# Kernel optimization log

Hardware: AMD Instinct MI355X
Metric: run time of the kernel (lower is better)

The kernel has to match this reference:

```python
import math
import jax, jax.numpy as jnp
import numpy as np
from jax import lax

PATCHSIZE = [(8, 8), (4, 4), (2, 2), (1, 1)]  # (width, height)
BN_EPS = 1e-5


def setup_inputs() -> dict:
    key = jax.random.key(0)
    ks = jax.random.split(key, 6)
    b, c, h, w = 4, 256, 64, 64
    s = 1.0 / math.sqrt(c)
    return {
        "x": jax.random.normal(ks[0], (b, c, h, w), jnp.float32),
        "Wq": jax.random.normal(ks[1], (c, c), jnp.float32) * s,
        "bq": jnp.zeros((c,), jnp.float32),
        "Wk": jax.random.normal(ks[2], (c, c), jnp.float32) * s,
        "bk": jnp.zeros((c,), jnp.float32),
        "Wv": jax.random.normal(ks[3], (c, c), jnp.float32) * s,
        "bv": jnp.zeros((c,), jnp.float32),
        "Wo": jax.random.normal(ks[4], (c, c, 3, 3), jnp.float32) * (1.0 / math.sqrt(c * 9)),
        "bo": jnp.zeros((c,), jnp.float32),
        "gamma": jnp.ones((c,), jnp.float32),
        "beta": jnp.zeros((c,), jnp.float32),
        "running_mean": jnp.zeros((c,), jnp.float32),
        "running_var": jnp.ones((c,), jnp.float32),
    }


def _patch_attention(q, k, v, ph, pw):
    # q/k/v: [b, dk, h, w] -> tokens [b, n_patches, dk*ph*pw]
    b, dk, h, w = q.shape
    oh, ow = h // ph, w // pw

    def to_tok(t):
        t = t.reshape(b, dk, oh, ph, ow, pw)
        return t.transpose(0, 2, 4, 1, 3, 5).reshape(b, oh * ow, dk * ph * pw)

    qt, kt, vt = to_tok(q), to_tok(k), to_tok(v)
    scale = 1.0 / math.sqrt(dk * ph * pw)
    scores = jnp.einsum("bnd,bmd->bnm", qt, kt) * scale
    y = jnp.einsum("bnm,bmd->bnd", jax.nn.softmax(scores, axis=-1), vt)
    y = y.reshape(b, oh, ow, dk, ph, pw).transpose(0, 3, 1, 4, 2, 5)
    return y.reshape(b, dk, h, w)


def reference(x, Wq, bq, Wk, bk, Wv, bv, Wo, bo, gamma, beta, running_mean, running_var):
    b, c, h, w = x.shape
    nh = len(PATCHSIZE)
    dk = c // nh
    # 1x1 conv QKV projections
    q = jnp.einsum("bchw,oc->bohw", x, Wq) + bq[:, None, None]
    k = jnp.einsum("bchw,oc->bohw", x, Wk) + bk[:, None, None]
    v = jnp.einsum("bchw,oc->bohw", x, Wv) + bv[:, None, None]
    outs = []
    for i, (pw_, ph_) in enumerate(PATCHSIZE):
        sl = slice(i * dk, (i + 1) * dk)
        outs.append(_patch_attention(q[:, sl], k[:, sl], v[:, sl], ph_, pw_))
    out = jnp.concatenate(outs, axis=1)
    # 3x3 conv, SAME padding
    out = lax.conv_general_dilated(
        out, Wo, window_strides=(1, 1), padding="SAME",
        dimension_numbers=("NCHW", "OIHW", "NCHW"),
    ) + bo[:, None, None]
    # BatchNorm2d (inference-mode with running stats)
    inv = lax.rsqrt(running_var + BN_EPS)
    out = (out - running_mean[:, None, None]) * (gamma * inv)[:, None, None] + beta[:, None, None]
    # LeakyReLU(0.2)
    return jnp.where(out >= 0, out, 0.2 * out)
```

## Files before the change

kernel.cpp:

```cpp
#include <hip/hip_runtime.h>
#include <hip/hip_bf16.h>
#include <math.h>

#define NPOS 4096
#define CPB  1048576
#define QOFF  ((size_t)0)
#define KOFF  ((size_t)4194304)
#define VOFF  ((size_t)8388608)
#define AOFF  ((size_t)12582912)
#define S0OFF ((size_t)16777216)
#define WTOFF ((size_t)21250048)
#define QTOFF   S0OFF
#define KTOFF   (S0OFF + (size_t)2097152)
#define SP0OFF  (S0OFF + (size_t)4194304)
#define VTOFF   QOFF
#define ML3OFF  (QOFF + (size_t)2097152)
#define ML2OFF  (QOFF + (size_t)2228224)
#define OP3OFF  KOFF
#define SP1OFF  VOFF
#define OP2OFF  (VOFF + (size_t)2097152)

#define LOG2E 1.44269504088896340736f

typedef __attribute__((ext_vector_type(8))) short bf16x8;
typedef __attribute__((ext_vector_type(4))) float f32x4;

static __device__ __forceinline__ unsigned short f2bf(float f) {
  __hip_bfloat16 h = __float2bfloat16(f);
  unsigned short u;
  __builtin_memcpy(&u, &h, sizeof(u));
  return u;
}

static __device__ __forceinline__ float bf2f(unsigned short u) {
  unsigned v = ((unsigned)u) << 16;
  float f;
  __builtin_memcpy(&f, &v, sizeof(f));
  return f;
}

template<int PH, int PW>
__device__ __forceinline__ void scat_qk(unsigned short* __restrict__ dst,
                                        const unsigned short* __restrict__ Ac,
                                        int gh, int tid) {
  constexpr int PP = PH * PW, OW = 64 / PW, D = 64 * PP;
  int po = gh / PH, y = gh % PH;
  constexpr int NCH = 64 * OW;
#pragma unroll
  for (int j = 0; j < NCH / 256; ++j) {
    int id = j * 256 + tid;
    int c = id / OW, qo = id % OW;
    int tt = po * OW + qo;
    unsigned short buf[PW];
#pragma unroll
    for (int x = 0; x < PW; ++x) buf[x] = Ac[c * 66 + qo * PW + x];
    unsigned short* dp = &dst[(size_t)tt * D + c * PP + y * PW];
    if constexpr (PW == 8)      { uint4 v;  __builtin_memcpy(&v, buf, 16); *(uint4*)dp = v; }
    else if constexpr (PW == 4) { uint2 v;  __builtin_memcpy(&v, buf, 8);  *(uint2*)dp = v; }
    else                        { unsigned v; __builtin_memcpy(&v, buf, 4); *(unsigned*)dp = v; }
  }
}

template<int PH, int PW>
__device__ __forceinline__ void scat_v(unsigned short* __restrict__ dst,
                                       const unsigned short* __restrict__ Ac,
                                       int gh, int tid) {
  constexpr int PP = PH * PW, OW = 64 / PW, NT = 4096 / PP;
  int po = gh / PH, y = gh % PH;
  constexpr int NCH = 64 * PW;
  constexpr int CPT = (NCH + 255) / 256;
#pragma unroll
  for (int j = 0; j < CPT; ++j) {
    int id = j * 256 + tid;
    if (NCH < 256 && id >= NCH) break;
    int c = id / PW, x = id % PW;
    int d = c * PP + y * PW + x;
    unsigned short* dp = &dst[(size_t)d * NT + po * OW];
#pragma unroll
    for (int s = 0; s < OW; s += 8) {
      unsigned short buf[8];
#pragma unroll
      for (int e = 0; e < 8; ++e) buf[e] = Ac[c * 66 + (s + e) * PW + x];
      uint4 v; __builtin_memcpy(&v, buf, 16);
      *(uint4*)&dp[s] = v;
    }
  }
}

__global__ __launch_bounds__(256) void qkv_fused(
    const float* __restrict__ x,
    const float* __restrict__ Wq, const float* __restrict__ Wk, const float* __restrict__ Wv,
    const float* __restrict__ bq, const float* __restrict__ bk, const float* __restrict__ bv,
    const float* __restrict__ Wo, unsigned short* __restrict__ W2,
    unsigned short* __restrict__ qt, unsigned short* __restrict__ kt_,
    unsigned short* __restrict__ vt) {
  if (blockIdx.z == 12) {
    int o = blockIdx.y * 64 + blockIdx.x;
    size_t base = (size_t)o * 2304;
#pragma unroll
    for (int r = 0; r < 9; ++r) {
      int rr = r * 256 + threadIdx.x;
      int c = rr / 9, k = rr % 9;
      W2[(size_t)k * 65536 + (size_t)o * 256 + c] = f2bf(Wo[base + rr]);
    }
    return;
  }
  int b = blockIdx.z / 3, t = blockIdx.z % 3;
  const float* W    = (t == 0) ? Wq : (t == 1) ? Wk : Wv;
  const float* bias = (t == 0) ? bq : (t == 1) ? bk : bv;
  int h = blockIdx.y, gh = blockIdx.x;
  int o0 = h * 64, p0 = gh * 64;
  __shared__ unsigned short smem[2 * 64 * 72];
  unsigned short* Wt = smem;
  unsigned short* Xs = smem + 64 * 72;
  int tid = threadIdx.x;
  int wv = tid >> 6, l = tid & 63;
  int lg = l >> 4, ll = l & 15;
  f32x4 acc[4];
#pragma unroll
  for (int mi = 0; mi < 4; ++mi) acc[mi] = (f32x4){0.f, 0.f, 0.f, 0.f};

  int wol = tid >> 2, wcp = (tid & 3) * 16;
  int xcc = tid >> 6, xpz = tid & 63;

  for (int c0 = 0; c0 < 256; c0 += 64) {
    __syncthreads();
#pragma unroll
    for (int u = 0; u < 4; ++u) {
      float4 w4 = *(const float4*)&W[(size_t)(o0 + wol) * 256 + c0 + wcp + u * 4];
      ushort4 pk;
      pk.x = f2bf(w4.x); pk.y = f2bf(w4.y); pk.z = f2bf(w4.z); pk.w = f2bf(w4.w);
      *(ushort4*)&Wt[wol * 72 + wcp + u * 4] = pk;
    }
#pragma unroll
    for (int r = 0; r < 16; ++r) {
      int c = xcc * 16 + r;
      Xs[xpz * 72 + c] = f2bf(x[(size_t)b * CPB + (size_t)(c0 + c) * NPOS + p0 + xpz]);
    }
    __syncthreads();
#pragma unroll
    for (int ks = 0; ks < 2; ++ks) {
      bf16x8 xb = *(const bf16x8*)&Xs[(wv * 16 + ll) * 72 + ks * 32 + lg * 8];
#pragma unroll
      for (int mi = 0; mi < 4; ++mi) {
        bf16x8 wa = *(const bf16x8*)&Wt[(mi * 16 + ll) * 72 + ks * 32 + lg * 8];
        acc[mi] = __builtin_amdgcn_mfma_f32_16x16x32_bf16(wa, xb, acc[mi], 0, 0, 0);
      }
    }
  }
  __syncthreads();
  float qs = 1.0f;
  if (t == 0) qs = (h == 2) ? 0.0625f * LOG2E : (h == 3) ? 0.125f * LOG2E : 1.0f;
  unsigned short* Ac = smem;
#pragma unroll
  for (int mi = 0; mi < 4; ++mi)
#pragma unroll
    for (int r = 0; r < 4; ++r) {
      int ol = mi * 16 + lg * 4 + r;
      Ac[ol * 66 + wv * 16 + ll] = f2bf((acc[mi][r] + bias[o0 + ol]) * qs);
    }
  __syncthreads();
  if (t < 2) {
    unsigned short* dst = (t == 0 ? qt : kt_) + ((size_t)b * 4 + h) * 262144;
    switch (h) {
      case 0: scat_qk<8, 8>(dst, Ac, gh, tid); break;
      case 1: scat_qk<4, 4>(dst, Ac, gh, tid); break;
      case 2: scat_qk<2, 2>(dst, Ac, gh, tid); break;
      default: {
        int p = tid >> 2, c0 = (tid & 3) * 16;
        unsigned short buf[16];
#pragma unroll
        for (int e = 0; e < 16; ++e) buf[e] = Ac[(c0 + e) * 66 + p];
        uint4 v0, v1;
        __builtin_memcpy(&v0, buf, 16);
        __builtin_memcpy(&v1, buf + 8, 16);
        uint4* d4 = (uint4*)&dst[(size_t)(gh * 64 + p) * 64 + c0];
        d4[0] = v0; d4[1] = v1;
      } break;
    }
  } else {
    unsigned short* dst = vt + ((size_t)b * 4 + h) * 262144;
    switch (h) {
      case 0: scat_v<8, 8>(dst, Ac, gh, tid); break;
      case 1: scat_v<4, 4>(dst, Ac, gh, tid); break;
      case 2: scat_v<2, 2>(dst, Ac, gh, tid); break;
      default: {
        if (tid < 64) {
#pragma unroll
          for (int seg = 0; seg < 8; ++seg) {
            unsigned short buf[8];
#pragma unroll
            for (int e = 0; e < 8; ++e) buf[e] = Ac[tid * 66 + seg * 8 + e];
            uint4 v; __builtin_memcpy(&v, buf, 16);
            *(uint4*)&dst[(size_t)tid * 4096 + gh * 64 + seg * 8] = v;
          }
        }
      } break;
    }
  }
}

template<int NTOK, int DDIM, int NSPLIT, int KVB, int PH, int PW, int HEAD>
__device__ __forceinline__ void flash_body(
    unsigned char* smem, int b, int q0, int split,
    const unsigned short* __restrict__ qt, const unsigned short* __restrict__ kt_,
    const unsigned short* __restrict__ vt, unsigned short* __restrict__ opart,
    float* __restrict__ ml, unsigned short* __restrict__ attbf) {
  constexpr int KSTR = DDIM + 8;
  constexpr int VSTR = KVB + 4;
  constexpr int NT   = KVB / 16;
  constexpr int KCH  = DDIM / 32;
  constexpr int PKS  = KVB / 32;
  constexpr int OCG  = DDIM / 16;
  constexpr int PP = PH * PW, OW = 64 / PW;
  const unsigned short* Q = qt + ((size_t)b * 4 + HEAD) * 262144;
  const unsigned short* K = kt_ + ((size_t)b * 4 + HEAD) * 262144;
  const unsigned short* V = vt + ((size_t)b * 4 + HEAD) * 262144;
  unsigned short* Ks = (unsigned short*)smem;
  unsigned short* Vs = Ks + KVB * KSTR;
  unsigned short* Psw = Vs + DDIM * VSTR;
  int tid = threadIdx.x;
  int wv = tid >> 6, l = tid & 63;
  int lg = l >> 4, ll = l & 15;
  int qw = q0 + wv * 16;
  unsigned short* Ps = Psw + wv * 16 * VSTR;

  bf16x8 qf[KCH];
#pragma unroll
  for (int kc = 0; kc < KCH; ++kc)
    qf[kc] = *(const bf16x8*)&Q[(size_t)(qw + ll) * DDIM + kc * 32 + lg * 8];

  bf16x8 onesf;
#pragma unroll
  for (int e = 0; e < 8; ++e) onesf[e] = (short)0x3F80;

  f32x4 lacc = (f32x4){0.f, 0.f, 0.f, 0.f};
  f32x4 o_acc[OCG];
#pragma unroll
  for (int c = 0; c < OCG; ++c) o_acc[c] = (f32x4){0.f, 0.f, 0.f, 0.f};

  for (int kt0 = split * (NTOK / NSPLIT); kt0 < (split + 1) * (NTOK / NSPLIT); kt0 += KVB) {
    __syncthreads();
#pragma unroll
    for (int i = 0; i < KVB * DDIM / 2048; ++i) {
      int u = i * 256 + tid;
      int key = u / (DDIM / 8), part = u % (DDIM / 8);
      *(uint4*)&Ks[key * KSTR + part * 8] =
          *(const uint4*)&K[(size_t)(kt0 + key) * DDIM + part * 8];
    }
#pragma unroll
    for (int i = 0; i < KVB * DDIM / 2048; ++i) {
      int u = i * 256 + tid;
      int d = u / (KVB / 8), part = u % (KVB / 8);
      *(uint4*)&Vs[d * VSTR + part * 8] =
          *(const uint4*)&V[(size_t)d * NTOK + kt0 + part * 8];
    }
    __syncthreads();
    f32x4 s_acc[NT];
#pragma unroll
    for (int n = 0; n < NT; ++n) s_acc[n] = (f32x4){0.f, 0.f, 0.f, 0.f};
    __builtin_amdgcn_s_setprio(1);
#pragma unroll
    for (int n = 0; n < NT; ++n)
#pragma unroll
      for (int kc = 0; kc < KCH; ++kc) {
        bf16x8 kf = *(const bf16x8*)&Ks[(n * 16 + ll) * KSTR + kc * 32 + lg * 8];
        s_acc[n] = __builtin_amdgcn_mfma_f32_16x16x32_bf16(qf[kc], kf, s_acc[n], 0, 0, 0);
      }
    __builtin_amdgcn_s_setprio(0);
#pragma unroll
    for (int n = 0; n < NT; ++n)
#pragma unroll
      for (int r = 0; r < 4; ++r)
        Ps[(lg * 4 + r) * VSTR + n * 16 + ll] = f2bf(exp2f(s_acc[n][r]));
    __builtin_amdgcn_s_setprio(1);
#pragma unroll
    for (int pk = 0; pk < PKS; ++pk) {
      bf16x8 pa = *(const bf16x8*)&Ps[ll * VSTR + pk * 32 + lg * 8];
      lacc = __builtin_amdgcn_mfma_f32_16x16x32_bf16(pa, onesf, lacc, 0, 0, 0);
#pragma unroll
      for (int c = 0; c < OCG; ++c) {
        bf16x8 vf = *(const bf16x8*)&Vs[(c * 16 + ll) * VSTR + pk * 32 + lg * 8];
        o_acc[c] = __builtin_amdgcn_mfma_f32_16x16x32_bf16(pa, vf, o_acc[c], 0, 0, 0);
      }
    }
    __builtin_amdgcn_s_setprio(0);
  }
  if constexpr (NSPLIT > 1) {
    size_t ob = (size_t)(b * NSPLIT + split) * NTOK;
#pragma unroll
    for (int r = 0; r < 4; ++r) {
      int q = qw + lg * 4 + r;
#pragma unroll
      for (int c = 0; c < OCG; ++c)
        opart[(ob + q) * DDIM + c * 16 + ll] = f2bf(o_acc[c][r]);
      if (ll == 0) {
        ml[(ob + q) * 2]     = 0.f;
        ml[(ob + q) * 2 + 1] = lacc[r];
      }
    }
  } else {
#pragma unroll
    for (int r = 0; r < 4; ++r) {
      float inv = 1.0f / lacc[r];
      int q = qw + lg * 4 + r;
      int po = q / OW, qo = q % OW;
#pragma unroll
      for (int c = 0; c < OCG; ++c) {
        int d = c * 16 + ll;
        int ch = d / PP, rem = d % PP, y = rem / PW, x = rem % PW;
        int pos = (po * PH + y) * 64 + qo * PW + x;
        attbf[((size_t)b * NPOS + pos) * 256 + HEAD * 64 + ch] = f2bf(o_acc[c][r] * inv);
      }
    }
  }
}

__device__ __forceinline__ void flash3_dbuf(
    unsigned char* smem, int b, int q0, int split,
    const unsigned short* __restrict__ qt, const unsigned short* __restrict__ kt_,
    const unsigned short* __restrict__ vt, unsigned short* __restrict__ opart,
    float* __restrict__ ml) {
  const unsigned short* Q = qt + ((size_t)b * 4 + 3) * 262144;
  const unsigned short* K = kt_ + ((size_t)b * 4 + 3) * 262144;
  const unsigned short* V = vt + ((size_t)b * 4 + 3) * 262144;
  int tid = threadIdx.x;
  int wv = tid >> 6, l = tid & 63;
  int lg = l >> 4, ll = l & 15;
  int qwA = q0 + wv * 16;
  int qwB = qwA + 64;
  unsigned short* Ps = (unsigned short*)(smem + 18432) + wv * 16 * 72;

  bf16x8 qfA[2], qfB[2];
  qfA[0] = *(const bf16x8*)&Q[(size_t)(qwA + ll) * 64 + lg * 8];
  qfA[1] = *(const bf16x8*)&Q[(size_t)(qwA + ll) * 64 + 32 + lg * 8];
  qfB[0] = *(const bf16x8*)&Q[(size_t)(qwB + ll) * 64 + lg * 8];
  qfB[1] = *(const bf16x8*)&Q[(size_t)(qwB + ll) * 64 + 32 + lg * 8];

  bf16x8 onesf;
#pragma unroll
  for (int e = 0; e < 8; ++e) onesf[e] = (short)0x3F80;

  f32x4 laccA = (f32x4){0.f, 0.f, 0.f, 0.f};
  f32x4 laccB = (f32x4){0.f, 0.f, 0.f, 0.f};
  f32x4 o_accA[4], o_accB[4];
#pragma unroll
  for (int c = 0; c < 4; ++c) {
    o_accA[c] = (f32x4){0.f, 0.f, 0.f, 0.f};
    o_accB[c] = (f32x4){0.f, 0.f, 0.f, 0.f};
  }

  const int kstart = split * 1024, kend = kstart + 1024;

  {
    unsigned short* Kd = (unsigned short*)smem;
#pragma unroll
    for (int i = 0; i < 2; ++i) {
      int u = i * 256 + tid, row = u >> 3, part = u & 7;
      *(uint4*)&Kd[row * 72 + part * 8] =
          *(const uint4*)&K[(size_t)(kstart + row) * 64 + part * 8];
    }
  }
  __syncthreads();

  int cur = 0;
  for (int kt0 = kstart; kt0 < kend; kt0 += 64) {
    const bool more = (kt0 + 64) < kend;
    if (more) {
      unsigned short* Kd = (unsigned short*)(smem + (cur ^ 1) * 9216);
#pragma unroll
      for (int i = 0; i < 2; ++i) {
        int u = i * 256 + tid, row = u >> 3, part = u & 7;
        *(uint4*)&Kd[row * 72 + part * 8] =
            *(const uint4*)&K[(size_t)(kt0 + 64 + row) * 64 + part * 8];
      }
    }
    unsigned short* Kc = (unsigned short*)(smem + cur * 9216);

    bf16x8 vfr[2][4];
#pragma unroll
    for (int pk = 0; pk < 2; ++pk)
#pragma unroll
      for (int c = 0; c < 4; ++c)
        vfr[pk][c] = *(const bf16x8*)&V[(size_t)(c * 16 + ll) * 4096 + kt0 + pk * 32 + lg * 8];
    bf16x8 kfr[4][2];
#pragma unroll
    for (int n = 0; n < 4; ++n)
#pragma unroll
      for (int kc = 0; kc < 2; ++kc)
        kfr[n][kc] = *(const bf16x8*)&Kc[(n * 16 + ll) * 72 + kc * 32 + lg * 8];

    {
      f32x4 s_acc[4];
#pragma unroll
      for (int n = 0; n < 4; ++n) s_acc[n] = (f32x4){0.f, 0.f, 0.f, 0.f};
      __builtin_amdgcn_s_setprio(1);
#pragma unroll
      for (int n = 0; n < 4; ++n)
#pragma unroll
        for (int kc = 0; kc < 2; ++kc)
          s_acc[n] = __builtin_amdgcn_mfma_f32_16x16x32_bf16(qfA[kc], kfr[n][kc], s_acc[n],
                                                             0, 0, 0);
      __builtin_amdgcn_s_setprio(0);
#pragma unroll
      for (int n = 0; n < 4; ++n)
#pragma unroll
        for (int r = 0; r < 4; ++r)
          Ps[(lg * 4 + r) * 72 + n * 16 + ll] = f2bf(exp2f(s_acc[n][r]));
      __builtin_amdgcn_s_setprio(1);
#pragma unroll
      for (int pk = 0; pk < 2; ++pk) {
        bf16x8 pa = *(const bf16x8*)&Ps[ll * 72 + pk * 32 + lg * 8];
        laccA = __builtin_amdgcn_mfma_f32_16x16x32_bf16(pa, onesf, laccA, 0, 0, 0);
#pragma unroll
        for (int c = 0; c < 4; ++c)
          o_accA[c] = __builtin_amdgcn_mfma_f32_16x16x32_bf16(pa, vfr[pk][c], o_accA[c],
                                                              0, 0, 0);
      }
      __builtin_amdgcn_s_setprio(0);
    }
    {
      f32x4 s_acc[4];
#pragma unroll
      for (int n = 0; n < 4; ++n) s_acc[n] = (f32x4){0.f, 0.f, 0.f, 0.f};
      __builtin_amdgcn_s_setprio(1);
#pragma unroll
      for (int n = 0; n < 4; ++n)
#pragma unroll
        for (int kc = 0; kc < 2; ++kc)
          s_acc[n] = __builtin_amdgcn_mfma_f32_16x16x32_bf16(qfB[kc], kfr[n][kc], s_acc[n],
                                                             0, 0, 0);
      __builtin_amdgcn_s_setprio(0);
#pragma unroll
      for (int n = 0; n < 4; ++n)
#pragma unroll
        for (int r = 0; r < 4; ++r)
          Ps[(lg * 4 + r) * 72 + n * 16 + ll] = f2bf(exp2f(s_acc[n][r]));
      __builtin_amdgcn_s_setprio(1);
#pragma unroll
      for (int pk = 0; pk < 2; ++pk) {
        bf16x8 pa = *(const bf16x8*)&Ps[ll * 72 + pk * 32 + lg * 8];
        laccB = __builtin_amdgcn_mfma_f32_16x16x32_bf16(pa, onesf, laccB, 0, 0, 0);
#pragma unroll
        for (int c = 0; c < 4; ++c)
          o_accB[c] = __builtin_amdgcn_mfma_f32_16x16x32_bf16(pa, vfr[pk][c], o_accB[c],
                                                              0, 0, 0);
      }
      __builtin_amdgcn_s_setprio(0);
    }
    __syncthreads();
    cur ^= 1;
  }
  size_t ob = (size_t)(b * 4 + split) * 4096;
#pragma unroll
  for (int r = 0; r < 4; ++r) {
    int qA = qwA + lg * 4 + r;
    int qB = qwB + lg * 4 + r;
#pragma unroll
    for (int c = 0; c < 4; ++c) {
      opart[(ob + qA) * 64 + c * 16 + ll] = f2bf(o_accA[c][r]);
      opart[(ob + qB) * 64 + c * 16 + ll] = f2bf(o_accB[c][r]);
    }
    if (ll == 0) {
      ml[(ob + qA) * 2]     = 0.f;
      ml[(ob + qA) * 2 + 1] = laccA[r];
      ml[(ob + qB) * 2]     = 0.f;
      ml[(ob + qB) * 2 + 1] = laccB[r];
    }
  }
}

__device__ __forceinline__ void h0_score_body(unsigned char* smem, int b, int ds,
                                              const unsigned short* __restrict__ qt,
                                              const unsigned short* __restrict__ kt_,
                                              float* __restrict__ spart) {
  const unsigned short* Q = qt + ((size_t)b * 4 + 0) * 262144;
  const unsigned short* K = kt_ + ((size_t)b * 4 + 0) * 262144;
  unsigned short* Qc = (unsigned short*)smem;
  unsigned short* Kc = Qc + 64 * 72;
  int tid = threadIdx.x;
  int wv = tid >> 6, l = tid & 63;
  int lg = l >> 4, ll = l & 15;
  f32x4 s_acc[4];
#pragma unroll
  for (int n = 0; n < 4; ++n) s_acc[n] = (f32x4){0.f, 0.f, 0.f, 0.f};
  for (int ch = 0; ch < 8; ++ch) {
    int d0 = ds * 512 + ch * 64;
    __syncthreads();
#pragma unroll
    for (int i = 0; i < 2; ++i) {
      int u = i * 256 + tid, row = u >> 3, part = u & 7;
      *(uint4*)&Qc[row * 72 + part * 8] = *(const uint4*)&Q[(size_t)row * 4096 + d0 + part * 8];
      *(uint4*)&Kc[row * 72 + part * 8] = *(const uint4*)&K[(size_t)row * 4096 + d0 + part * 8];
    }
    __syncthreads();
#pragma unroll
    for (int n = 0; n < 4; ++n)
#pragma unroll
      for (int ks = 0; ks < 2; ++ks) {
        bf16x8 qa = *(const bf16x8*)&Qc[(wv * 16 + ll) * 72 + ks * 32 + lg * 8];
        bf16x8 kf = *(const bf16x8*)&Kc[(n * 16 + ll) * 72 + ks * 32 + lg * 8];
        s_acc[n] = __builtin_amdgcn_mfma_f32_16x16x32_bf16(qa, kf, s_acc[n], 0, 0, 0);
      }
  }
#pragma unroll
  for (int n = 0; n < 4; ++n)
#pragma unroll
    for (int r = 0; r < 4; ++r)
      spart[(((size_t)b * 8 + ds) * 64 + (wv * 16 + lg * 4 + r)) * 64 + n * 16 + ll] =
          s_acc[n][r];
}

__device__ __forceinline__ void h1_score_body(unsigned char* smem, int b, int qtile, int ds,
                                              const unsigned short* __restrict__ qt,
                                              const unsigned short* __restrict__ kt_,
                                              float* __restrict__ spart) {
  int q0 = qtile * 64, dbase = ds * 128;
  const unsigned short* Q = qt + ((size_t)b * 4 + 1) * 262144;
  const unsigned short* K = kt_ + ((size_t)b * 4 + 1) * 262144;
  unsigned short* Qc = (unsigned short*)smem;
  unsigned short* Kc = Qc + 64 * 72;
  int tid = threadIdx.x;
  int wv = tid >> 6, l = tid & 63;
  int lg = l >> 4, ll = l & 15;
  f32x4 s_acc[16];
#pragma unroll
  for (int n = 0; n < 16; ++n) s_acc[n] = (f32x4){0.f, 0.f, 0.f, 0.f};
  for (int dc = 0; dc < 2; ++dc) {
    int d0 = dbase + dc * 64;
    for (int kh = 0; kh < 2; ++kh) {
      __syncthreads();
      if (kh == 0) {
#pragma unroll
        for (int i = 0; i < 2; ++i) {
          int u = i * 256 + tid, row = u >> 3, part = u & 7;
          *(uint4*)&Qc[row * 72 + part * 8] =
              *(const uint4*)&Q[(size_t)(q0 + row) * 1024 + d0 + part * 8];
        }
      }
#pragma unroll
      for (int i = 0; i < 4; ++i) {
        int u = i * 256 + tid, row = u >> 3, part = u & 7;
        *(uint4*)&Kc[row * 72 + part * 8] =
            *(const uint4*)&K[(size_t)(kh * 128 + row) * 1024 + d0 + part * 8];
      }
      __syncthreads();
#pragma unroll
      for (int ks = 0; ks < 2; ++ks) {
        bf16x8 qa = *(const bf16x8*)&Qc[(wv * 16 + ll) * 72 + ks * 32 + lg * 8];
#pragma unroll
        for (int nn = 0; nn < 8; ++nn) {
          bf16x8 kf = *(const bf16x8*)&Kc[(nn * 16 + ll) * 72 + ks * 32 + lg * 8];
          s_acc[kh * 8 + nn] = __builtin_amdgcn_mfma_f32_16x16x32_bf16(qa, kf, s_acc[kh * 8 + nn],
                                                                      0, 0, 0);
        }
      }
    }
  }
#pragma unroll
  for (int n = 0; n < 16; ++n)
#pragma unroll
    for (int r = 0; r < 4; ++r) {
      int q = q0 + wv * 16 + lg * 4 + r;
      spart[(((size_t)b * 8 + ds) * 256 + q) * 256 + n * 16 + ll] = s_acc[n][r];
    }
}

__global__ __launch_bounds__(256) void attn_all(
    const unsigned short* __restrict__ qt, const unsigned short* __restrict__ kt_,
    const unsigned short* __restrict__ vt,
    unsigned short* __restrict__ op2, float* __restrict__ ml2,
    unsigned short* __restrict__ op3, float* __restrict__ ml3,
    float* __restrict__ sp0, float* __restrict__ sp1,
    unsigned short* __restrict__ attbf) {
  __shared__ __align__(16) unsigned char smem[39936];
  int bid = blockIdx.x;
  if (bid < 512) {
    int b = bid & 3, qy = (bid >> 2) & 31, split = bid >> 7;
    flash3_dbuf(smem, b, qy * 128, split, qt, kt_, vt, op3, ml3);
  } else if (bid < 640) {
    int r = bid - 512;
    int b = r & 3, qy = (r >> 2) & 15, split = r >> 6;
    flash_body<1024, 256, 2, 32, 2, 2, 2>(smem, b, qy * 64, split, qt, kt_, vt,
                                          op2, ml2, attbf);
  } else {
    int r = bid - 640;
    if (r < 32) h0_score_body(smem, r >> 3, r & 7, qt, kt_, sp0);
    else {
      int rr = r - 32;
      h1_score_body(smem, rr >> 5, (rr >> 3) & 3, rr & 7, qt, kt_, sp1);
    }
  }
}

__device__ __forceinline__ void h0_pv_body(unsigned char* smem, int b, int ds,
                                           const float* __restrict__ spart,
                                           const unsigned short* __restrict__ vt,
                                           unsigned short* __restrict__ attbf) {
  const unsigned short* V = vt + ((size_t)b * 4 + 0) * 262144;
  float* S = (float*)smem;
  unsigned short* Ps = (unsigned short*)(smem + 16640);
  unsigned short* Vc = Ps + 64 * 72;
  int tid = threadIdx.x;
  int wv = tid >> 6, l = tid & 63;
  int lg = l >> 4, ll = l & 15;
#pragma unroll
  for (int i = 0; i < 16; ++i) {
    int idx = i * 256 + tid, q = idx >> 6, k = idx & 63;
    float s = 0.f;
#pragma unroll
    for (int sl = 0; sl < 8; ++sl)
      s += spart[(((size_t)b * 8 + sl) * 64 + q) * 64 + k];
    S[q * 65 + k] = s;
  }
  __syncthreads();
  for (int rr = 0; rr < 16; ++rr) {
    int row = wv * 16 + rr;
    float v = S[row * 65 + l] * 0.015625f;
    float m = v;
#pragma unroll
    for (int d = 32; d >= 1; d >>= 1) m = fmaxf(m, __shfl_xor(m, d));
    float p = __expf(v - m);
    float su = p;
#pragma unroll
    for (int d = 32; d >= 1; d >>= 1) su += __shfl_xor(su, d);
    Ps[row * 72 + l] = f2bf(p / su);
  }
  __syncthreads();
  for (int ch = 0; ch < 8; ++ch) {
    int d0 = ds * 512 + ch * 64;
    __syncthreads();
#pragma unroll
    for (int i = 0; i < 2; ++i) {
      int u = i * 256 + tid, row = u >> 3, part = u & 7;
      *(uint4*)&Vc[row * 72 + part * 8] =
          *(const uint4*)&V[(size_t)(d0 + row) * 64 + part * 8];
    }
    __syncthreads();
    f32x4 o[4];
#pragma unroll
    for (int cg = 0; cg < 4; ++cg) o[cg] = (f32x4){0.f, 0.f, 0.f, 0.f};
#pragma unroll
    for (int cg = 0; cg < 4; ++cg)
#pragma unroll
      for (int ks = 0; ks < 2; ++ks) {
        bf16x8 pa = *(const bf16x8*)&Ps[(wv * 16 + ll) * 72 + ks * 32 + lg * 8];
        bf16x8 vf = *(const bf16x8*)&Vc[(cg * 16 + ll) * 72 + ks * 32 + lg * 8];
        o[cg] = __builtin_amdgcn_mfma_f32_16x16x32_bf16(pa, vf, o[cg], 0, 0, 0);
      }
#pragma unroll
    for (int cg = 0; cg < 4; ++cg)
#pragma unroll
      for (int r = 0; r < 4; ++r) {
        int q = wv * 16 + lg * 4 + r;
        int d = d0 + cg * 16 + ll;
        int c = d >> 6, rem = d & 63, y = rem >> 3, x = rem & 7;
        int po = q >> 3, qo = q & 7;
        int pos = (po * 8 + y) * 64 + qo * 8 + x;
        attbf[((size_t)b * NPOS + pos) * 256 + c] = f2bf(o[cg][r]);
      }
  }
}

__device__ __forceinline__ void h1_pv_body(unsigned char* smem, int b, int qtile, int vs,
                                           const float* __restrict__ spart,
                                           const unsigned short* __restrict__ vt,
                                           unsigned short* __restrict__ attbf) {
  int q0 = qtile * 64, dv0 = vs * 128;
  const unsigned short* V = vt + ((size_t)b * 4 + 1) * 262144;
  unsigned short* Ps = (unsigned short*)smem;
  unsigned short* Vs = Ps + 64 * 264;
  int tid = threadIdx.x;
  int wv = tid >> 6, l = tid & 63;
  int lg = l >> 4, ll = l & 15;
  for (int rr = 0; rr < 16; ++rr) {
    int row = q0 + wv * 16 + rr;
    float sv[4];
#pragma unroll
    for (int c4 = 0; c4 < 4; ++c4) {
      float s = 0.f;
#pragma unroll
      for (int sl = 0; sl < 8; ++sl)
        s += spart[(((size_t)b * 8 + sl) * 256 + row) * 256 + c4 * 64 + l];
      sv[c4] = s * 0.03125f;
    }
    float m = fmaxf(fmaxf(sv[0], sv[1]), fmaxf(sv[2], sv[3]));
#pragma unroll
    for (int d = 32; d >= 1; d >>= 1) m = fmaxf(m, __shfl_xor(m, d));
    float p[4], su = 0.f;
#pragma unroll
    for (int c4 = 0; c4 < 4; ++c4) { p[c4] = __expf(sv[c4] - m); su += p[c4]; }
#pragma unroll
    for (int d = 32; d >= 1; d >>= 1) su += __shfl_xor(su, d);
    float inv = 1.0f / su;
#pragma unroll
    for (int c4 = 0; c4 < 4; ++c4)
      Ps[(wv * 16 + rr) * 264 + c4 * 64 + l] = f2bf(p[c4] * inv);
  }
  for (int vc = 0; vc < 4; ++vc) {
    int d0 = dv0 + vc * 32;
    __syncthreads();
#pragma unroll
    for (int i = 0; i < 4; ++i) {
      int u = i * 256 + tid, row = u >> 5, part = u & 31;
      *(uint4*)&Vs[row * 264 + part * 8] =
          *(const uint4*)&V[(size_t)(d0 + row) * 256 + part * 8];
    }
    __syncthreads();
    f32x4 o[2];
    o[0] = (f32x4){0.f, 0.f, 0.f, 0.f};
    o[1] = (f32x4){0.f, 0.f, 0.f, 0.f};
#pragma unroll
    for (int ks = 0; ks < 8; ++ks) {
      bf16x8 pa = *(const bf16x8*)&Ps[(wv * 16 + ll) * 264 + ks * 32 + lg * 8];
#pragma unroll
      for (int cg = 0; cg < 2; ++cg) {
        bf16x8 vf = *(const bf16x8*)&Vs[(cg * 16 + ll) * 264 + ks * 32 + lg * 8];
        o[cg] = __builtin_amdgcn_mfma_f32_16x16x32_bf16(pa, vf, o[cg], 0, 0, 0);
      }
    }
#pragma unroll
    for (int cg = 0; cg < 2; ++cg)
#pragma unroll
      for (int r = 0; r < 4; ++r) {
        int q = q0 + wv * 16 + lg * 4 + r;
        int d = d0 + cg * 16 + ll;
        int c = d >> 4, rem = d & 15, y = rem >> 2, x = rem & 3;
        int po = q >> 4, qo = q & 15;
        int pos = (po * 4 + y) * 64 + qo * 4 + x;
        attbf[((size_t)b * NPOS + pos) * 256 + 64 + c] = f2bf(o[cg][r]);
      }
  }
}

__global__ __launch_bounds__(256) void finish_all(
    const float* __restrict__ sp0, const float* __restrict__ sp1,
    const unsigned short* __restrict__ op2, const float* __restrict__ ml2,
    const unsigned short* __restrict__ op3, const float* __restrict__ ml3,
    const unsigned short* __restrict__ vt, unsigned short* __restrict__ attbf) {
  __shared__ __align__(16) unsigned char smem[50688];
  int bid = blockIdx.x;
  if (bid < 32) { h0_pv_body(smem, bid >> 3, bid & 7, sp0, vt, attbf); return; }
  if (bid < 160) {
    int r = bid - 32;
    h1_pv_body(smem, r >> 5, (r >> 3) & 3, r & 7, sp1, vt, attbf);
    return;
  }
  int cb = bid - 160;
  if (cb < 4096) {
    int b = cb >> 10, q = cb & 1023;
    int d = threadIdx.x;
    float num = 0.f, den = 0.f;
#pragma unroll
    for (int s = 0; s < 2; ++s) {
      den += ml2[((size_t)(b * 2 + s) * 1024 + q) * 2 + 1];
      num += bf2f(op2[((size_t)(b * 2 + s) * 1024 + q) * 256 + d]);
    }
    int c = d >> 2, rem = d & 3, y = rem >> 1, x = rem & 1;
    int po = q >> 5, qo = q & 31;
    int pos = (po * 2 + y) * 64 + qo * 2 + x;
    attbf[((size_t)b * NPOS + pos) * 256 + 128 + c] = f2bf(num / den);
  } else {
    cb -= 4096;
    int b = cb >> 10, qt4 = cb & 1023;
    int q = qt4 * 4 + (threadIdx.x >> 6), ch = threadIdx.x & 63;
    float num = 0.f, den = 0.f;
#pragma unroll
    for (int s = 0; s < 4; ++s) {
      den += ml3[((size_t)(b * 4 + s) * 4096 + q) * 2 + 1];
      num += bf2f(op3[((size_t)(b * 4 + s) * 4096 + q) * 64 + ch]);
    }
    attbf[((size_t)b * 4096 + q) * 256 + 192 + ch] = f2bf(num / den);
  }
}

__global__ __launch_bounds__(512) void conv_mfma(
    const unsigned short* __restrict__ attbf, const unsigned short* __restrict__ w2,
    const float* __restrict__ bo, const float* __restrict__ gamma,
    const float* __restrict__ beta, const float* __restrict__ rmean,
    const float* __restrict__ rvar, float* __restrict__ out) {
  int hq = blockIdx.x, ot = blockIdx.y, b = blockIdx.z;
  int h0 = hq * 4, o0 = ot * 64;
  __shared__ unsigned short As[4 * 66 * 72];
  __shared__ unsigned short Ws[3 * 64 * 72];
  int tid = threadIdx.x;
  int wi = tid >> 6, l = tid & 63;
  int hrow = wi >> 1, wseg = wi & 1;
  int lg = l >> 4, ll = l & 15;
  const size_t attb = (size_t)b * NPOS * 256;
  f32x4 acc[4][2];
#pragma unroll
  for (int mi = 0; mi < 4; ++mi)
#pragma unroll
    for (int ni = 0; ni < 2; ++ni) acc[mi][ni] = (f32x4){0.f, 0.f, 0.f, 0.f};

  for (int dy = 0; dy < 3; ++dy) {
    for (int c0 = 0; c0 < 256; c0 += 64) {
      __syncthreads();
      if (tid < 256) {
        int rowl = tid >> 6, w = tid & 63;
        int ghh = h0 + dy - 1 + rowl;
        uint4 z = make_uint4(0u, 0u, 0u, 0u);
        uint4 a[8];
        if (ghh >= 0 && ghh < 64) {
          const uint4* src = (const uint4*)(attbf + attb + ((size_t)(ghh * 64 + w) * 256 + c0));
#pragma unroll
          for (int q = 0; q < 8; ++q) a[q] = src[q];
        } else {
#pragma unroll
          for (int q = 0; q < 8; ++q) a[q] = z;
        }
        uint4* dst = (uint4*)&As[(rowl * 66 + 1 + w) * 72];
#pragma unroll
        for (int q = 0; q < 8; ++q) dst[q] = a[q];
        if (w == 0 || w == 63) {
          uint4* dz = (uint4*)&As[(rowl * 66 + ((w == 0) ? 0 : 65)) * 72];
#pragma unroll
          for (int q = 0; q < 8; ++q) dz[q] = z;
        }
      } else {
        int p = tid - 256;
        int dx = p >> 6, ol = p & 63;
        if (dx < 3) {
          const uint4* src = (const uint4*)(w2 + ((size_t)(dy * 3 + dx) * 65536 +
                                                  (size_t)(o0 + ol) * 256 + c0));
          uint4* dst = (uint4*)&Ws[(dx * 64 + ol) * 72];
#pragma unroll
          for (int q = 0; q < 8; ++q) dst[q] = src[q];
        }
      }
      __syncthreads();
#pragma unroll
      for (int dx = 0; dx < 3; ++dx) {
#pragma unroll
        for (int ks = 0; ks < 2; ++ks) {
          bf16x8 af[4];
#pragma unroll
          for (int mi = 0; mi < 4; ++mi)
            af[mi] = *(const bf16x8*)&Ws[(dx * 64 + mi * 16 + ll) * 72 + ks * 32 + lg * 8];
#pragma unroll
          for (int ni = 0; ni < 2; ++ni) {
            bf16x8 bfr = *(const bf16x8*)&As[(hrow * 66 + wseg * 32 + ni * 16 + ll + dx) * 72 +
                                             ks * 32 + lg * 8];
#pragma unroll
            for (int mi = 0; mi < 4; ++mi)
              acc[mi][ni] = __builtin_amdgcn_mfma_f32_16x16x32_bf16(af[mi], bfr, acc[mi][ni],
                                                                    0, 0, 0);
          }
        }
      }
    }
  }
  int h = h0 + hrow;
#pragma unroll
  for (int mi = 0; mi < 4; ++mi) {
#pragma unroll
    for (int r = 0; r < 4; ++r) {
      int o = o0 + mi * 16 + lg * 4 + r;
      float g  = gamma[o] * rsqrtf(rvar[o] + 1e-5f);
      float bb = (bo[o] - rmean[o]) * g + beta[o];
#pragma unroll
      for (int ni = 0; ni < 2; ++ni) {
        float zv = acc[mi][ni][r] * g + bb;
        zv = (zv >= 0.f) ? zv : 0.2f * zv;
        out[((size_t)(b * 256 + o)) * NPOS + h * 64 + wseg * 32 + ni * 16 + ll] = zv;
      }
    }
  }
}

extern "C" void kernel_launch(void* const* d_in, const int* in_sizes, int n_in,
                              void* d_out, int out_size, void* d_ws, size_t ws_size,
                              hipStream_t stream) {
  (void)in_sizes; (void)n_in; (void)out_size; (void)ws_size;
  const float* x     = (const float*)d_in[0];
  const float* Wq    = (const float*)d_in[1];
  const float* bq    = (const float*)d_in[2];
  const float* Wk    = (const float*)d_in[3];
  const float* bk    = (const float*)d_in[4];
  const float* Wv    = (const float*)d_in[5];
  const float* bv    = (const float*)d_in[6];
  const float* Wo    = (const float*)d_in[7];
  const float* bo    = (const float*)d_in[8];
  const float* gamma = (const float*)d_in[9];
  const float* beta  = (const float*)d_in[10];
  const float* rmean = (const float*)d_in[11];
  const float* rvar  = (const float*)d_in[12];
  float* ws  = (float*)d_ws;
  float* out = (float*)d_out;
  unsigned short* attbf = (unsigned short*)(ws + AOFF);
  unsigned short* w2bf  = (unsigned short*)(ws + WTOFF);
  unsigned short* qt    = (unsigned short*)(ws + QTOFF);
  unsigned short* kt    = (unsigned short*)(ws + KTOFF);
  unsigned short* vt    = (unsigned short*)(ws + VTOFF);
  unsigned short* op2   = (unsigned short*)(ws + OP2OFF);
  unsigned short* op3   = (unsigned short*)(ws + OP3OFF);

  qkv_fused<<<dim3(64, 4, 13), 256, 0, stream>>>(x, Wq, Wk, Wv, bq, bk, bv,
                                                 Wo, w2bf, qt, kt, vt);

  attn_all<<<800, 256, 0, stream>>>(qt, kt, vt,
                                    op2, ws + ML2OFF,
                                    op3, ws + ML3OFF,
                                    ws + SP0OFF, ws + SP1OFF, attbf);

  finish_all<<<8352, 256, 0, stream>>>(ws + SP0OFF, ws + SP1OFF,
                                       op2, ws + ML2OFF,
                                       op3, ws + ML3OFF, vt, attbf);

  conv_mfma<<<dim3(16, 4, 4), 512, 0, stream>>>(attbf, w2bf, bo, gamma, beta,
                                                rmean, rvar, out);
}
```

Measured before the change: 211.0 us.

## Stage V tiles through double-buffered XOR-swizzled LDS in head-3 flash kernel

V fragments for the head-3 flash attention path were previously read directly from global memory each iteration. They are now loaded cooperatively into LDS alongside K, double-buffered with the K prefetch. K, V and the P scratch tiles move from padded 72-element rows to 128-byte rows with an XOR swizzle to avoid bank conflicts. LDS use grows slightly, which may affect occupancy for the shared attn_all kernel.

After: 200.2 us. 5.1% less time.

```diff
diff --git a/kernel.cpp b/kernel.cpp
--- a/kernel.cpp
+++ b/kernel.cpp
@@ -329,7 +329,7 @@
   int lg = l >> 4, ll = l & 15;
   int qwA = q0 + wv * 16;
   int qwB = qwA + 64;
-  unsigned short* Ps = (unsigned short*)(smem + 18432) + wv * 16 * 72;
+  unsigned char* Psb = smem + 32768 + wv * 16 * 128;
 
   bf16x8 qfA[2], qfB[2];
   qfA[0] = *(const bf16x8*)&Q[(size_t)(qwA + ll) * 64 + lg * 8];
@@ -353,12 +353,16 @@
   const int kstart = split * 1024, kend = kstart + 1024;
 
   {
-    unsigned short* Kd = (unsigned short*)smem;
+    unsigned char* Kd = smem;
+    unsigned char* Vd = smem + 8192;
 #pragma unroll
     for (int i = 0; i < 2; ++i) {
       int u = i * 256 + tid, row = u >> 3, part = u & 7;
-      *(uint4*)&Kd[row * 72 + part * 8] =
+      int sw = (part ^ (row & 7)) * 16;
+      *(uint4*)(Kd + row * 128 + sw) =
           *(const uint4*)&K[(size_t)(kstart + row) * 64 + part * 8];
+      *(uint4*)(Vd + row * 128 + sw) =
+          *(const uint4*)&V[(size_t)row * 4096 + kstart + part * 8];
     }
   }
   __syncthreads();
@@ -367,28 +371,34 @@
   for (int kt0 = kstart; kt0 < kend; kt0 += 64) {
     const bool more = (kt0 + 64) < kend;
     if (more) {
-      unsigned short* Kd = (unsigned short*)(smem + (cur ^ 1) * 9216);
+      unsigned char* Kd = smem + (cur ^ 1) * 16384;
+      unsigned char* Vd = Kd + 8192;
 #pragma unroll
       for (int i = 0; i < 2; ++i) {
         int u = i * 256 + tid, row = u >> 3, part = u & 7;
-        *(uint4*)&Kd[row * 72 + part * 8] =
+        int sw = (part ^ (row & 7)) * 16;
+        *(uint4*)(Kd + row * 128 + sw) =
             *(const uint4*)&K[(size_t)(kt0 + 64 + row) * 64 + part * 8];
-      }
-    }
-    unsigned short* Kc = (unsigned short*)(smem + cur * 9216);
-
-    bf16x8 vfr[2][4];
+        *(uint4*)(Vd + row * 128 + sw) =
+            *(const uint4*)&V[(size_t)row * 4096 + (kt0 + 64) + part * 8];
+      }
+    }
+    unsigned char* Kc = smem + cur * 16384;
+    unsigned char* Vc = Kc + 8192;
+
+    bf16x8 kfr[4][2], vfr[2][4];
+#pragma unroll
+    for (int n = 0; n < 4; ++n)
+#pragma unroll
+      for (int kc = 0; kc < 2; ++kc)
+        kfr[n][kc] = *(const bf16x8*)(Kc + (n * 16 + ll) * 128 +
+                                      (((kc * 4 + lg) ^ (ll & 7)) * 16));
 #pragma unroll
     for (int pk = 0; pk < 2; ++pk)
 #pragma unroll
       for (int c = 0; c < 4; ++c)
-        vfr[pk][c] = *(const bf16x8*)&V[(size_t)(c * 16 + ll) * 4096 + kt0 + pk * 32 + lg * 8];
-    bf16x8 kfr[4][2];
-#pragma unroll
-    for (int n = 0; n < 4; ++n)
-#pragma unroll
-      for (int kc = 0; kc < 2; ++kc)
-        kfr[n][kc] = *(const bf16x8*)&Kc[(n * 16 + ll) * 72 + kc * 32 + lg * 8];
+        vfr[pk][c] = *(const bf16x8*)(Vc + (c * 16 + ll) * 128 +
+                                      (((pk * 4 + lg) ^ (ll & 7)) * 16));
 
     {
       f32x4 s_acc[4];
@@ -405,12 +415,15 @@
 #pragma unroll
       for (int n = 0; n < 4; ++n)
 #pragma unroll
-        for (int r = 0; r < 4; ++r)
-          Ps[(lg * 4 + r) * 72 + n * 16 + ll] = f2bf(exp2f(s_acc[n][r]));
+        for (int r = 0; r < 4; ++r) {
+          int prow = lg * 4 + r;
+          int slot = (((n * 2 + (ll >> 3)) ^ (prow & 7)) << 3) + (ll & 7);
+          *(unsigned short*)(Psb + prow * 128 + slot * 2) = f2bf(exp2f(s_acc[n][r]));
+        }
       __builtin_amdgcn_s_setprio(1);
 #pragma unroll
       for (int pk = 0; pk < 2; ++pk) {
-        bf16x8 pa = *(const bf16x8*)&Ps[ll * 72 + pk * 32 + lg * 8];
+        bf16x8 pa = *(const bf16x8*)(Psb + ll * 128 + (((pk * 4 + lg) ^ (ll & 7)) * 16));
         laccA = __builtin_amdgcn_mfma_f32_16x16x32_bf16(pa, onesf, laccA, 0, 0, 0);
 #pragma unroll
         for (int c = 0; c < 4; ++c)
@@ -434,12 +447,15 @@
 #pragma unroll
       for (int n = 0; n < 4; ++n)
 #pragma unroll
-        for (int r = 0; r < 4; ++r)
-          Ps[(lg * 4 + r) * 72 + n * 16 + ll] = f2bf(exp2f(s_acc[n][r]));
+        for (int r = 0; r < 4; ++r) {
+          int prow = lg * 4 + r;
+          int slot = (((n * 2 + (ll >> 3)) ^ (prow & 7)) << 3) + (ll & 7);
+          *(unsigned short*)(Psb + prow * 128 + slot * 2) = f2bf(exp2f(s_acc[n][r]));
+        }
       __builtin_amdgcn_s_setprio(1);
 #pragma unroll
       for (int pk = 0; pk < 2; ++pk) {
-        bf16x8 pa = *(const bf16x8*)&Ps[ll * 72 + pk * 32 + lg * 8];
+        bf16x8 pa = *(const bf16x8*)(Psb + ll * 128 + (((pk * 4 + lg) ^ (ll & 7)) * 16));
         laccB = __builtin_amdgcn_mfma_f32_16x16x32_bf16(pa, onesf, laccB, 0, 0, 0);
 #pragma unroll
         for (int c = 0; c < 4; ++c)
@@ -573,7 +589,7 @@
     unsigned short* __restrict__ op3, float* __restrict__ ml3,
     float* __restrict__ sp0, float* __restrict__ sp1,
     unsigned short* __restrict__ attbf) {
-  __shared__ __align__(16) unsigned char smem[39936];
+  __shared__ __align__(16) unsigned char smem[40960];
   int bid = blockIdx.x;
   if (bid < 512) {
     int b = bid & 3, qy = (bid >> 2) & 31, split = bid >> 7;
```
